# Kernel tuning notes

Hardware: AMD Instinct MI355X
Metric: run time of the kernel (lower is better)

## Reference

```python
import jax, jax.numpy as jnp
import numpy as np
import math

D = 1024
H = 16

def _new_gelu(x):
    return 0.5 * x * (1.0 + jnp.tanh(math.sqrt(2.0 / math.pi) * (x + 0.044715 * x ** 3)))

def _layer_norm(x, w):
    mu = jnp.mean(x, axis=-1, keepdims=True)
    var = jnp.var(x, axis=-1, keepdims=True)
    return (x - mu) * jax.lax.rsqrt(var + 1e-5) * w

def setup_inputs() -> dict:
    key = jax.random.key(0)
    ks = jax.random.split(key, 8)
    B, T = 2, 2048
    s = lambda fan_in: 1.0 / math.sqrt(fan_in)
    return {
        "x": jax.random.normal(ks[0], (B, T, D), jnp.float32),
        "ln1_w": jnp.ones((D,), jnp.float32),
        "attn_w": jax.random.normal(ks[1], (D, 3 * D), jnp.float32) * s(D),
        "attn_b": jnp.zeros((3 * D,), jnp.float32),
        "proj_w": jax.random.normal(ks[2], (D, D), jnp.float32) * s(D),
        "proj_b": jnp.zeros((D,), jnp.float32),
        "ln2_w": jnp.ones((D,), jnp.float32),
        "li1_w": jax.random.normal(ks[3], (D, 4 * D), jnp.float32) * s(D),
        "li1_b": jnp.zeros((4 * D,), jnp.float32),
        "li2_w": jax.random.normal(ks[4], (4 * D, D), jnp.float32) * s(4 * D),
        "li2_b": jnp.zeros((D,), jnp.float32),
    }

def reference(x, ln1_w, attn_w, attn_b, proj_w, proj_b, ln2_w, li1_w, li1_b, li2_w, li2_b):
    B, T, C = x.shape
    Dh = C // H
    # --- causal self-attention on pre-LN input ---
    h = _layer_norm(x, ln1_w)
    qkv = h @ attn_w + attn_b                      # [B,T,3C]
    q, k, v = jnp.split(qkv, 3, axis=-1)
    q = q.reshape(B, T, H, Dh)
    k = k.reshape(B, T, H, Dh)
    v = v.reshape(B, T, H, Dh)
    # NOTE: faithful to source — scale is 1/sqrt(BATCH), not 1/sqrt(head_dim)
    scale = 1.0 / math.sqrt(B)
    scores = jnp.einsum('bthd,bshd->bhts', q, k) * scale   # [B,H,T,T]
    causal = jnp.tril(jnp.ones((T, T), bool))
    scores = jnp.where(causal, scores, -jnp.inf)
    attn = jax.nn.softmax(scores, axis=-1)
    o = jnp.einsum('bhts,bshd->bthd', attn, v).reshape(B, T, C)
    x = x + o @ proj_w + proj_b
    # --- MLP ---
    h = _layer_norm(x, ln2_w)
    x = x + _new_gelu(h @ li1_w + li1_b) @ li2_w + li2_b
    return x
```

## Files before the change

kernel.cpp:

```cpp
#include <hip/hip_runtime.h>

typedef _Float16 f16;
typedef _Float16 f16x8 __attribute__((ext_vector_type(8)));
typedef _Float16 f16x4 __attribute__((ext_vector_type(4)));
typedef float    f32x4 __attribute__((ext_vector_type(4)));
typedef float    f32x16 __attribute__((ext_vector_type(16)));
typedef unsigned u32;
typedef unsigned u32x4 __attribute__((ext_vector_type(4)));

#define GAS __attribute__((address_space(1)))
#define LAS __attribute__((address_space(3)))

template <int N> struct IC { static constexpr int v = N; };

static __device__ __forceinline__ void gload_lds16(const void* g, void* l) {
    __builtin_amdgcn_global_load_lds((const GAS void*)g, (LAS void*)l, 16, 0, 0);
}

__global__ void wconv_t(const float* __restrict__ w, f16* __restrict__ wt, int K, int N) {
    __shared__ f16 t[32][33];
    const int tx = threadIdx.x, ty = threadIdx.y;
    const int n0 = blockIdx.x * 32, k0 = blockIdx.y * 32;
#pragma unroll
    for (int i = 0; i < 4; i++)
        t[ty + i * 8][tx] = (f16)w[(size_t)(k0 + ty + i * 8) * N + n0 + tx];
    __syncthreads();
#pragma unroll
    for (int i = 0; i < 4; i++)
        wt[(size_t)(n0 + ty + i * 8) * K + k0 + tx] = t[tx][ty + i * 8];
}

__global__ __launch_bounds__(256) void ln_kernel(const float* __restrict__ x,
                                                 const float* __restrict__ w,
                                                 f16* __restrict__ h) {
    const int row = blockIdx.x, tid = threadIdx.x;
    const float4 v = reinterpret_cast<const float4*>(x)[(size_t)row * 256 + tid];
    float s = v.x + v.y + v.z + v.w;
    float q = v.x * v.x + v.y * v.y + v.z * v.z + v.w * v.w;
#pragma unroll
    for (int m = 1; m < 64; m <<= 1) { s += __shfl_xor(s, m); q += __shfl_xor(q, m); }
    __shared__ float ss[4], qq[4];
    if ((tid & 63) == 0) { ss[tid >> 6] = s; qq[tid >> 6] = q; }
    __syncthreads();
    s = ss[0] + ss[1] + ss[2] + ss[3];
    q = qq[0] + qq[1] + qq[2] + qq[3];
    const float mu = s * (1.0f / 1024.0f);
    const float var = q * (1.0f / 1024.0f) - mu * mu;
    const float rs = rsqrtf(var + 1e-5f);
    const float4 wv = reinterpret_cast<const float4*>(w)[tid];
    f16x4 o;
    o[0] = (f16)((v.x - mu) * rs * wv.x);
    o[1] = (f16)((v.y - mu) * rs * wv.y);
    o[2] = (f16)((v.z - mu) * rs * wv.z);
    o[3] = (f16)((v.w - mu) * rs * wv.w);
    reinterpret_cast<f16x4*>(h)[(size_t)row * 256 + tid] = o;
}

__global__ __launch_bounds__(256) void vtrans(const f16* __restrict__ V, f16* __restrict__ Vt) {
    __shared__ f16 tl[64][72];
    const int tid = threadIdx.x;
    const int t0 = blockIdx.x * 64, bh = blockIdx.y;
    const int b = bh >> 4, hh = bh & 15;
    const int rr = tid >> 3, cc = (tid & 7) * 8;
#pragma unroll
    for (int p = 0; p < 2; p++) {
        f16x8 v = *(const f16x8*)(V + (size_t)(b * 2048 + t0 + p * 32 + rr) * 1024 + hh * 64 + cc);
#pragma unroll
        for (int j = 0; j < 8; j++) tl[p * 32 + rr][cc + j] = v[j];
    }
    __syncthreads();
#pragma unroll
    for (int p = 0; p < 2; p++) {
        const int d = p * 32 + rr;
        f16x8 o;
#pragma unroll
        for (int j = 0; j < 8; j++) o[j] = tl[cc + j][d];
        *(f16x8*)(Vt + (size_t)(bh * 64 + d) * 2048 + t0 + cc) = o;
    }
}

template <int EPI>
static __device__ __forceinline__ void gemm_epi(
    int gr, int gc, float v, int N, int gx,
    const float* bias, const float* res, void* outp,
    f16* oq, f16* ok, f16* ov, int bz, int BM) {
    if (EPI == 0) {
        if (gc < 1024)      oq[(size_t)gr * 1024 + gc]        = (f16)(v * 0.70710678118654752f);
        else if (gc < 2048) ok[(size_t)gr * 1024 + gc - 1024] = (f16)v;
        else                ov[(size_t)gr * 1024 + gc - 2048] = (f16)v;
    } else if (EPI == 1) {
        ((float*)outp)[(size_t)gr * N + gc] = v + res[(size_t)gr * N + gc];
    } else if (EPI == 2) {
        const float z = 0.7978845608028654f * (v + 0.044715f * v * v * v);
        const float t = 1.0f - 2.0f / (__builtin_amdgcn_exp2f(2.8853900817779268f * z) + 1.0f);
        ((f16*)outp)[(size_t)gr * N + gc] = (f16)(0.5f * v * (1.0f + t));
    } else {
        float* P = (float*)outp + (size_t)bz * ((size_t)gx * BM) * N;
        P[(size_t)gr * N + gc] = v;
    }
}

template <int EPI>
__global__ __launch_bounds__(512, 2) void gemm256(
    const f16* __restrict__ A, int lda,
    const f16* __restrict__ Bt, int ldb,
    const float* __restrict__ bias,
    const float* __restrict__ res,
    void* __restrict__ outp,
    f16* __restrict__ oq, f16* __restrict__ ok, f16* __restrict__ ov,
    int N, int K) {
    __shared__ alignas(16) f16 pool[8 * 8192];
    const int tid = threadIdx.x;
    const int lane = tid & 63, wv = tid >> 6;
    const int wr = wv >> 2, wc = wv & 3;
    const int m0 = blockIdx.x * 256, n0 = blockIdx.y * 256;
    const int l15 = lane & 15, lg = lane >> 4;
    const int swz = l15 & 7;

    f32x4 acc[8][4] = {};
    f16x8 bf[4][2];

    const int gcol16 = (tid & 7) ^ ((tid >> 3) & 7);
    const f16* aSrc[2][2];
    const f16* bSrc[2][2];
#pragma unroll
    for (int c = 0; c < 2; c++) {
        const int lr = c * 64 + (tid >> 3);
#pragma unroll
        for (int h = 0; h < 2; h++) {
            const int ar = ((lr >> 5) << 6) + h * 32 + (lr & 31);
            aSrc[c][h] = A + (size_t)(m0 + ar) * lda + gcol16 * 8;
            const int br = ((lr >> 6) << 7) + h * 64 + (lr & 63);
            bSrc[c][h] = Bt + (size_t)(n0 + br) * ldb + gcol16 * 8;
        }
    }
    f16* ldst = pool + tid * 8;

    auto stageQ = [&](int par, int qid, int kt) {
        f16* d = ldst + (par * 4 + qid) * 8192;
        if (qid >= 2) {
            gload_lds16(aSrc[0][qid - 2] + kt * 64, d);
            gload_lds16(aSrc[1][qid - 2] + kt * 64, d + 4096);
        } else {
            gload_lds16(bSrc[0][qid] + kt * 64, d);
            gload_lds16(bSrc[1][qid] + kt * 64, d + 4096);
        }
    };

    auto loadB = [&](int par) {
        const f16* bb = pool + par * 32768 + (wc & 1) * 8192 + (wc >> 1) * 4096 + l15 * 64;
#pragma unroll
        for (int ni = 0; ni < 4; ni++)
#pragma unroll
            for (int kk = 0; kk < 2; kk++)
                bf[ni][kk] = *(const f16x8*)(bb + ni * 1024 + (((kk * 4 + lg) ^ swz) * 8));
    };
    auto computeQ = [&](int par, auto qc) {
        constexpr int Q = decltype(qc)::v;
        const f16* ab = pool + par * 32768 + (2 + (Q & 1)) * 8192
                        + wr * 4096 + (Q >> 1) * 2048 + l15 * 64;
        f16x8 af[2][2];
#pragma unroll
        for (int mi2 = 0; mi2 < 2; mi2++)
#pragma unroll
            for (int kk = 0; kk < 2; kk++)
                af[mi2][kk] = *(const f16x8*)(ab + mi2 * 1024 + (((kk * 4 + lg) ^ swz) * 8));
        __builtin_amdgcn_s_setprio(1);
#pragma unroll
        for (int mi2 = 0; mi2 < 2; mi2++)
#pragma unroll
            for (int ni = 0; ni < 4; ni++)
#pragma unroll
                for (int kk = 0; kk < 2; kk++)
                    acc[Q * 2 + mi2][ni] = __builtin_amdgcn_mfma_f32_16x16x32_f16(
                        af[mi2][kk], bf[ni][kk], acc[Q * 2 + mi2][ni], 0, 0, 0);
        __builtin_amdgcn_s_setprio(0);
    };

#define VMW(n) asm volatile("s_waitcnt vmcnt(" #n ")" ::: "memory"); __builtin_amdgcn_s_barrier()

    const int nt = K >> 6;
    stageQ(0, 0, 0); stageQ(0, 1, 0); stageQ(0, 2, 0); stageQ(0, 3, 0);
    stageQ(1, 0, 1);
    VMW(6);

    for (int kt = 0; kt < nt - 2; ++kt) {
        const int par = kt & 1, parn = par ^ 1;
        stageQ(parn, 1, kt + 1); VMW(6); loadB(par); computeQ(par, IC<0>{});
        stageQ(parn, 2, kt + 1); VMW(6); computeQ(par, IC<1>{});
        stageQ(parn, 3, kt + 1); VMW(6); computeQ(par, IC<2>{});
        stageQ(par, 0, kt + 2);  VMW(6); computeQ(par, IC<3>{});
    }
    {
        const int kt = nt - 2, par = kt & 1, parn = par ^ 1;
        stageQ(parn, 1, kt + 1); VMW(6); loadB(par); computeQ(par, IC<0>{});
        stageQ(parn, 2, kt + 1); VMW(6); computeQ(par, IC<1>{});
        stageQ(parn, 3, kt + 1); VMW(6); computeQ(par, IC<2>{});
        VMW(4); computeQ(par, IC<3>{});
    }
    {
        const int par = (nt - 1) & 1;
        VMW(2); loadB(par); computeQ(par, IC<0>{});
        VMW(0); computeQ(par, IC<1>{});
        computeQ(par, IC<2>{});
        computeQ(par, IC<3>{});
    }
#undef VMW

#pragma unroll
    for (int mi = 0; mi < 8; mi++)
#pragma unroll
        for (int ni = 0; ni < 4; ni++) {
            const int gc = n0 + wc * 64 + ni * 16 + l15;
            const float bb = (EPI == 3) ? 0.0f : bias[gc];
#pragma unroll
            for (int r = 0; r < 4; r++) {
                const int gr = m0 + wr * 128 + mi * 16 + lg * 4 + r;
                gemm_epi<EPI>(gr, gc, acc[mi][ni][r] + bb, N, gridDim.x,
                              bias, res, outp, oq, ok, ov, blockIdx.z, 256);
            }
        }
}

template <int EPI>
__global__ __launch_bounds__(512) void gemm128(
    const f16* __restrict__ A, int lda,
    const f16* __restrict__ Bt, int ldb,
    const float* __restrict__ bias,
    const float* __restrict__ res,
    void* __restrict__ outp,
    f16* __restrict__ oq, f16* __restrict__ ok, f16* __restrict__ ov,
    int N, int K) {
    __shared__ alignas(16) f16 As[3][128 * 32];
    __shared__ alignas(16) f16 Bs[3][128 * 32];
    const int tid = threadIdx.x;
    const int lane = tid & 63, wv = tid >> 6;
    const int wr = wv >> 2, wc = wv & 3;
    const int m0 = blockIdx.x * 128, n0 = blockIdx.y * 128;
    const int l15 = lane & 15, lg = lane >> 4;

    f32x4 acc[4][2] = {};

    const int ar = tid >> 2;
    const int ac = (tid & 3) * 8;
    const size_t koff = (size_t)blockIdx.z * K;
    const f16* gA = A + (size_t)(m0 + ar) * lda + ac + koff;
    const f16* gB = Bt + (size_t)(n0 + ar) * ldb + ac + koff;
    char* lA0 = (char*)As + wv * 1024;
    char* lB0 = (char*)Bs + wv * 1024;

    auto stage = [&](int buf, int k0) {
        gload_lds16(gA + k0, lA0 + buf * 8192);
        gload_lds16(gB + k0, lB0 + buf * 8192);
    };
    auto compute = [&](int buf) {
        f16x8 af[4], bf[2];
#pragma unroll
        for (int i = 0; i < 4; i++)
            af[i] = *(const f16x8*)&As[buf][(wr * 64 + i * 16 + l15) * 32 + lg * 8];
#pragma unroll
        for (int n = 0; n < 2; n++)
            bf[n] = *(const f16x8*)&Bs[buf][(wc * 32 + n * 16 + l15) * 32 + lg * 8];
#pragma unroll
        for (int mi = 0; mi < 4; mi++)
#pragma unroll
            for (int ni = 0; ni < 2; ni++)
                acc[mi][ni] = __builtin_amdgcn_mfma_f32_16x16x32_f16(af[mi], bf[ni], acc[mi][ni], 0, 0, 0);
    };

    const int nk = K >> 5;
    stage(0, 0);
    if (nk > 1) {
        stage(1, 32);
        asm volatile("s_waitcnt vmcnt(2)" ::: "memory");
    } else {
        asm volatile("s_waitcnt vmcnt(0)" ::: "memory");
    }
    __builtin_amdgcn_s_barrier();

    for (int t = 0; t < nk; ++t) {
        const bool pref = (t + 2 < nk);
        if (pref) stage((t + 2) % 3, (t + 2) * 32);
        compute(t % 3);
        if (t + 1 < nk) {
            if (pref) asm volatile("s_waitcnt vmcnt(2)" ::: "memory");
            else      asm volatile("s_waitcnt vmcnt(0)" ::: "memory");
            __builtin_amdgcn_s_barrier();
        }
    }

#pragma unroll
    for (int mi = 0; mi < 4; mi++)
#pragma unroll
        for (int ni = 0; ni < 2; ni++) {
            const int gc = n0 + wc * 32 + ni * 16 + l15;
            const float bb = (EPI == 3) ? 0.0f : bias[gc];
#pragma unroll
            for (int r = 0; r < 4; r++) {
                const int gr = m0 + wr * 64 + mi * 16 + lg * 4 + r;
                gemm_epi<EPI>(gr, gc, acc[mi][ni][r] + bb, N, gridDim.x,
                              bias, res, outp, oq, ok, ov, blockIdx.z, 128);
            }
        }
}

__global__ __launch_bounds__(256) void kred(const float* __restrict__ p0,
                                            const float* __restrict__ p1,
                                            const float* __restrict__ bias,
                                            const float* __restrict__ res,
                                            float* __restrict__ out) {
    const size_t i = (size_t)blockIdx.x * 256 + threadIdx.x;
    const float4 a = ((const float4*)p0)[i];
    const float4 b = ((const float4*)p1)[i];
    const float4 r = ((const float4*)res)[i];
    const float4 w = ((const float4*)bias)[i & 255];
    float4 o;
    o.x = a.x + b.x + r.x + w.x;
    o.y = a.y + b.y + r.y + w.y;
    o.z = a.z + b.z + r.z + w.z;
    o.w = a.w + b.w + r.w + w.w;
    ((float4*)out)[i] = o;
}

__global__ __launch_bounds__(512) void attn_kernel(
    const f16* __restrict__ Q, const f16* __restrict__ Kb,
    const f16* __restrict__ Vt, f16* __restrict__ O) {
    __shared__ alignas(16) char pool[32768];
    const int tid = threadIdx.x, lane = tid & 63, w = tid >> 6;
    const int l31 = lane & 31, hi = lane >> 5;
    const int bx = blockIdx.x;
    const int qs = bx >> 5, bh = bx & 31;
    const int b = bh >> 4, hh = bh & 15;
    const int qtile = w * 8 + qs;
    const int q0 = qtile * 32;
    const int last = qtile >> 1;
    const int nk = ((56 + qs) >> 1) + 1;

    const f16* qrow = Q + (size_t)(b * 2048 + q0 + l31) * 1024 + hh * 64 + hi * 8;
    f16x8 qf[4];
#pragma unroll
    for (int s = 0; s < 4; s++) qf[s] = *(const f16x8*)(qrow + s * 16);

    f32x16 oacc[2] = {};
    float m = -3e38f, l = 0.0f;

    const int srow = tid >> 3, sslot = (tid & 7) ^ ((tid >> 3) & 7);
    const f16* kg = Kb + ((size_t)b * 2048 + srow) * 1024 + hh * 64 + sslot * 8;
    const f16* vg = Vt + ((size_t)bh * 64 + srow) * 2048 + sslot * 8;
    char* kld = pool + tid * 16;
    char* vld = pool + 8192 + tid * 16;

    auto stage = [&](int buf, int kt) {
        gload_lds16(kg + (size_t)kt * 65536, kld + buf * 16384);
        gload_lds16(vg + kt * 64, vld + buf * 16384);
    };

    const int rs = l31 & 7;

    auto tilestep = [&](int buf, bool diag) {
        const f16* Kbuf = (const f16*)(pool + buf * 16384);
        const f16* Vbuf = (const f16*)(pool + buf * 16384 + 8192);
        const bool doH1 = !diag || (qtile & 1);
        const int triH = qtile & 1;

        f16x8 k0[4], k1[4];
#pragma unroll
        for (int s = 0; s < 4; s++)
            k0[s] = *(const f16x8*)&Kbuf[l31 * 64 + (((s * 2 + hi) ^ rs) * 8)];
        if (doH1)
#pragma unroll
            for (int s = 0; s < 4; s++)
                k1[s] = *(const f16x8*)&Kbuf[(32 + l31) * 64 + (((s * 2 + hi) ^ rs) * 8)];

        f32x16 sacc0 = {}, sacc1 = {};
        __builtin_amdgcn_s_setprio(1);
#pragma unroll
        for (int s = 0; s < 4; s++)
            sacc0 = __builtin_amdgcn_mfma_f32_32x32x16_f16(k0[s], qf[s], sacc0, 0, 0, 0);
        if (doH1)
#pragma unroll
            for (int s = 0; s < 4; s++)
                sacc1 = __builtin_amdgcn_mfma_f32_32x32x16_f16(k1[s], qf[s], sacc1, 0, 0, 0);
        __builtin_amdgcn_s_setprio(0);

        if (diag) {
            if (triH == 0) {
#pragma unroll
                for (int r = 0; r < 16; r++) {
                    const int keyoff = (r & 3) + 8 * (r >> 2) + 4 * hi;
                    sacc0[r] = (keyoff > l31) ? -3e38f : sacc0[r];
                }
            } else {
#pragma unroll
                for (int r = 0; r < 16; r++) {
                    const int keyoff = (r & 3) + 8 * (r >> 2) + 4 * hi;
                    sacc1[r] = (keyoff > l31) ? -3e38f : sacc1[r];
                }
            }
        }
        float t8[8];
#pragma unroll
        for (int i = 0; i < 8; i++) t8[i] = fmaxf(sacc0[2 * i], sacc0[2 * i + 1]);
        if (doH1)
#pragma unroll
            for (int i = 0; i < 8; i++) t8[i] = fmaxf(t8[i], fmaxf(sacc1[2 * i], sacc1[2 * i + 1]));
#pragma unroll
        for (int i = 0; i < 4; i++) t8[i] = fmaxf(t8[i], t8[i + 4]);
        float tm = fmaxf(fmaxf(t8[0], t8[1]), fmaxf(t8[2], t8[3]));
        tm = fmaxf(tm, __shfl_xor(tm, 32));
        const bool up = tm > m + 8.0f;
        if (__any(up)) {
            const float mnew = up ? tm : m;
            const float alpha = __expf(m - mnew);
            m = mnew;
            l *= alpha;
#pragma unroll
            for (int r = 0; r < 16; r++) { oacc[0][r] *= alpha; oacc[1][r] *= alpha; }
        }
        const float mref = m * 1.44269504f;

        float psum = 0.0f;
        u32 wd[8];
        {
            float p[16];
#pragma unroll
            for (int r = 0; r < 16; r++)
                p[r] = __builtin_amdgcn_exp2f(sacc0[r] * 1.44269504f - mref);
            float s8[8];
#pragma unroll
            for (int i = 0; i < 8; i++) s8[i] = p[2 * i] + p[2 * i + 1];
#pragma unroll
            for (int i = 0; i < 4; i++) s8[i] = s8[i] + s8[i + 4];
            psum += (s8[0] + s8[1]) + (s8[2] + s8[3]);
#pragma unroll
            for (int i = 0; i < 8; i++)
                wd[i] = __builtin_bit_cast(u32, __builtin_amdgcn_cvt_pkrtz(p[2 * i], p[2 * i + 1]));
        }
        const u32 e0 = __shfl_xor(hi ? wd[0] : wd[2], 32);
        const u32 e1 = __shfl_xor(hi ? wd[1] : wd[3], 32);
        const u32 e2 = __shfl_xor(hi ? wd[4] : wd[6], 32);
        const u32 e3 = __shfl_xor(hi ? wd[5] : wd[7], 32);
        u32x4 c0, c1;
        c0[0] = hi ? e0 : wd[0]; c0[1] = hi ? e1 : wd[1];
        c0[2] = hi ? wd[2] : e0; c0[3] = hi ? wd[3] : e1;
        c1[0] = hi ? e2 : wd[4]; c1[1] = hi ? e3 : wd[5];
        c1[2] = hi ? wd[6] : e2; c1[3] = hi ? wd[7] : e3;
        const f16x8 pb00 = __builtin_bit_cast(f16x8, c0);
        const f16x8 pb01 = __builtin_bit_cast(f16x8, c1);

        f16x8 vfa, vfb;
        __builtin_amdgcn_s_setprio(1);
        vfa = *(const f16x8*)&Vbuf[l31 * 64 + ((hi ^ rs) * 8)];
        vfb = *(const f16x8*)&Vbuf[l31 * 64 + (((2 + hi) ^ rs) * 8)];
        oacc[0] = __builtin_amdgcn_mfma_f32_32x32x16_f16(vfa, pb00, oacc[0], 0, 0, 0);
        oacc[0] = __builtin_amdgcn_mfma_f32_32x32x16_f16(vfb, pb01, oacc[0], 0, 0, 0);
        vfa = *(const f16x8*)&Vbuf[(32 + l31) * 64 + ((hi ^ rs) * 8)];
        vfb = *(const f16x8*)&Vbuf[(32 + l31) * 64 + (((2 + hi) ^ rs) * 8)];
        oacc[1] = __builtin_amdgcn_mfma_f32_32x32x16_f16(vfa, pb00, oacc[1], 0, 0, 0);
        oacc[1] = __builtin_amdgcn_mfma_f32_32x32x16_f16(vfb, pb01, oacc[1], 0, 0, 0);
        __builtin_amdgcn_s_setprio(0);

        if (doH1) {
            float p[16];
#pragma unroll
            for (int r = 0; r < 16; r++)
                p[r] = __builtin_amdgcn_exp2f(sacc1[r] * 1.44269504f - mref);
            float s8[8];
#pragma unroll
            for (int i = 0; i < 8; i++) s8[i] = p[2 * i] + p[2 * i + 1];
#pragma unroll
            for (int i = 0; i < 4; i++) s8[i] = s8[i] + s8[i + 4];
            psum += (s8[0] + s8[1]) + (s8[2] + s8[3]);
#pragma unroll
            for (int i = 0; i < 8; i++)
                wd[i] = __builtin_bit_cast(u32, __builtin_amdgcn_cvt_pkrtz(p[2 * i], p[2 * i + 1]));
            const u32 f0 = __shfl_xor(hi ? wd[0] : wd[2], 32);
            const u32 f1 = __shfl_xor(hi ? wd[1] : wd[3], 32);
            const u32 f2 = __shfl_xor(hi ? wd[4] : wd[6], 32);
            const u32 f3 = __shfl_xor(hi ? wd[5] : wd[7], 32);
            u32x4 d0, d1;
            d0[0] = hi ? f0 : wd[0]; d0[1] = hi ? f1 : wd[1];
            d0[2] = hi ? wd[2] : f0; d0[3] = hi ? wd[3] : f1;
            d1[0] = hi ? f2 : wd[4]; d1[1] = hi ? f3 : wd[5];
            d1[2] = hi ? wd[6] : f2; d1[3] = hi ? wd[7] : f3;
            const f16x8 pb10 = __builtin_bit_cast(f16x8, d0);
            const f16x8 pb11 = __builtin_bit_cast(f16x8, d1);

            __builtin_amdgcn_s_setprio(1);
            vfa = *(const f16x8*)&Vbuf[l31 * 64 + (((4 + hi) ^ rs) * 8)];
            vfb = *(const f16x8*)&Vbuf[l31 * 64 + (((6 + hi) ^ rs) * 8)];
            oacc[0] = __builtin_amdgcn_mfma_f32_32x32x16_f16(vfa, pb10, oacc[0], 0, 0, 0);
            oacc[0] = __builtin_amdgcn_mfma_f32_32x32x16_f16(vfb, pb11, oacc[0], 0, 0, 0);
            vfa = *(const f16x8*)&Vbuf[(32 + l31) * 64 + (((4 + hi) ^ rs) * 8)];
            vfb = *(const f16x8*)&Vbuf[(32 + l31) * 64 + (((6 + hi) ^ rs) * 8)];
            oacc[1] = __builtin_amdgcn_mfma_f32_32x32x16_f16(vfa, pb10, oacc[1], 0, 0, 0);
            oacc[1] = __builtin_amdgcn_mfma_f32_32x32x16_f16(vfb, pb11, oacc[1], 0, 0, 0);
            __builtin_amdgcn_s_setprio(0);
        }
        psum += __shfl_xor(psum, 32);
        l += psum;
    };

    stage(0, 0);
    asm volatile("s_waitcnt vmcnt(0)" ::: "memory");
    __builtin_amdgcn_s_barrier();
    int buf = 0;
    for (int t = 0; t < nk; ++t) {
        if (t + 1 < nk) stage(buf ^ 1, t + 1);
        if (t <= last) tilestep(buf, t == last);
        asm volatile("s_waitcnt vmcnt(0)" ::: "memory");
        __builtin_amdgcn_s_barrier();
        buf ^= 1;
    }

    const float inv = 1.0f / l;
    f16* ot = (f16*)pool + (w & 3) * (32 * 72);
#pragma unroll
    for (int g = 0; g < 2; g++) {
        if ((w >> 2) == g) {
#pragma unroll
            for (int dt = 0; dt < 2; dt++)
#pragma unroll
                for (int r = 0; r < 16; r++) {
                    const int d = dt * 32 + (r & 3) + 8 * (r >> 2) + 4 * hi;
                    ot[l31 * 72 + d] = (f16)(oacc[dt][r] * inv);
                }
            asm volatile("s_waitcnt lgkmcnt(0)" ::: "memory");
#pragma unroll
            for (int i = 0; i < 4; i++) {
                const int row = i * 8 + (lane >> 3), col = (lane & 7) * 8;
                const f16x8 o8 = *(const f16x8*)&ot[row * 72 + col];
                *(f16x8*)(O + (size_t)(b * 2048 + q0 + row) * 1024 + hh * 64 + col) = o8;
            }
        }
        __syncthreads();
    }
}

extern "C" void kernel_launch(void* const* d_in, const int* in_sizes, int n_in,
                              void* d_out, int out_size, void* d_ws, size_t ws_size,
                              hipStream_t stream) {
    const float* x      = (const float*)d_in[0];
    const float* ln1_w  = (const float*)d_in[1];
    const float* attn_w = (const float*)d_in[2];
    const float* attn_b = (const float*)d_in[3];
    const float* proj_w = (const float*)d_in[4];
    const float* proj_b = (const float*)d_in[5];
    const float* ln2_w  = (const float*)d_in[6];
    const float* li1_w  = (const float*)d_in[7];
    const float* li1_b  = (const float*)d_in[8];
    const float* li2_w  = (const float*)d_in[9];
    const float* li2_b  = (const float*)d_in[10];
    float* out = (float*)d_out;

    char* ws = (char*)d_ws;
    size_t off = 0;
    auto alloc = [&](size_t bytes) { void* p = ws + off; off += (bytes + 255) & ~(size_t)255; return p; };
    f16* W1t = (f16*)alloc((size_t)3072 * 1024 * 2);
    f16* W2t = (f16*)alloc((size_t)1024 * 1024 * 2);
    f16* W3t = (f16*)alloc((size_t)4096 * 1024 * 2);
    f16* W4t = (f16*)alloc((size_t)1024 * 4096 * 2);
    f16* h   = (f16*)alloc((size_t)4096 * 1024 * 2);
    f16* Qb  = (f16*)alloc((size_t)4096 * 1024 * 2);
    f16* Kb  = (f16*)alloc((size_t)4096 * 1024 * 2);
    f16* Vb  = (f16*)alloc((size_t)4096 * 1024 * 2);
    f16* Vt  = (f16*)alloc((size_t)4096 * 1024 * 2);
    f16* Ob  = (f16*)alloc((size_t)4096 * 1024 * 2);
    float* x1 = (float*)alloc((size_t)4096 * 1024 * 4);
    float* P  = (float*)alloc((size_t)2 * 4096 * 1024 * 4);
    f16* Ab = Qb;

    dim3 b328(32, 8);
    wconv_t<<<dim3(96, 32),  b328, 0, stream>>>(attn_w, W1t, 1024, 3072);
    wconv_t<<<dim3(32, 32),  b328, 0, stream>>>(proj_w, W2t, 1024, 1024);
    wconv_t<<<dim3(128, 32), b328, 0, stream>>>(li1_w,  W3t, 1024, 4096);
    wconv_t<<<dim3(32, 128), b328, 0, stream>>>(li2_w,  W4t, 4096, 1024);

    ln_kernel<<<4096, 256, 0, stream>>>(x, ln1_w, h);
    gemm256<0><<<dim3(16, 12), 512, 0, stream>>>(h, 1024, W1t, 1024, attn_b, nullptr,
                                                 nullptr, Qb, Kb, Vb, 3072, 1024);
    vtrans<<<dim3(32, 32), 256, 0, stream>>>(Vb, Vt);
    attn_kernel<<<256, 512, 0, stream>>>(Qb, Kb, Vt, Ob);
    gemm128<1><<<dim3(32, 8), 512, 0, stream>>>(Ob, 1024, W2t, 1024, proj_b, x,
                                                x1, nullptr, nullptr, nullptr, 1024, 1024);
    ln_kernel<<<4096, 256, 0, stream>>>(x1, ln2_w, h);
    gemm256<2><<<dim3(16, 16), 512, 0, stream>>>(h, 1024, W3t, 1024, li1_b, nullptr,
                                                 Ab, nullptr, nullptr, nullptr, 4096, 1024);
    gemm128<3><<<dim3(32, 8, 2), 512, 0, stream>>>(Ab, 4096, W4t, 4096, nullptr, nullptr,
                                                   P, nullptr, nullptr, nullptr, 1024, 2048);
    kred<<<4096, 256, 0, stream>>>(P, P + (size_t)4096 * 1024, li2_b, x1, out);
}
```

Measured before the change: 246.3 us.

## Software-pipeline LDS fragment reads one quarter ahead of MFMA in gemm256

Restructures the gemm256 main loop so the A and B fragments for the next quarter (and the next k-tile's first quarter) are read from LDS before the current quarter's MFMAs issue. Global-to-LDS staging now runs three quarters ahead instead of one. LDS read latency is meant to hide behind matrix math rather than stall each quarter. This costs extra registers for the double-buffered fragments (bfN, afE, afO) under launch_bounds(512,2), and adds lgkmcnt(0) waits at every barrier.

After: 247.8 us. No clear change (+0.6%).

```diff
diff --git a/kernel.cpp b/kernel.cpp
--- a/kernel.cpp
+++ b/kernel.cpp
@@ -118,7 +118,7 @@
     const int swz = l15 & 7;
 
     f32x4 acc[8][4] = {};
-    f16x8 bf[4][2];
+    f16x8 bf[4][2], bfN[2][2], afE[2][2], afO[2][2];
 
     const int gcol16 = (tid & 7) ^ ((tid >> 3) & 7);
     const f16* aSrc[2][2];
@@ -147,24 +147,34 @@
         }
     };
 
-    auto loadB = [&](int par) {
+    auto rdBF01 = [&](int par, f16x8 (*dst)[2]) {
         const f16* bb = pool + par * 32768 + (wc & 1) * 8192 + (wc >> 1) * 4096 + l15 * 64;
 #pragma unroll
-        for (int ni = 0; ni < 4; ni++)
+        for (int ni = 0; ni < 2; ni++)
+#pragma unroll
+            for (int kk = 0; kk < 2; kk++)
+                dst[ni][kk] = *(const f16x8*)(bb + ni * 1024 + (((kk * 4 + lg) ^ swz) * 8));
+    };
+    auto rdBF23 = [&](int par) {
+        const f16* bb = pool + par * 32768 + (wc & 1) * 8192 + (wc >> 1) * 4096 + l15 * 64;
+#pragma unroll
+        for (int ni = 2; ni < 4; ni++)
 #pragma unroll
             for (int kk = 0; kk < 2; kk++)
                 bf[ni][kk] = *(const f16x8*)(bb + ni * 1024 + (((kk * 4 + lg) ^ swz) * 8));
     };
-    auto computeQ = [&](int par, auto qc) {
+    auto rdAF = [&](auto qc, int par, f16x8 (&af)[2][2]) {
         constexpr int Q = decltype(qc)::v;
         const f16* ab = pool + par * 32768 + (2 + (Q & 1)) * 8192
                         + wr * 4096 + (Q >> 1) * 2048 + l15 * 64;
-        f16x8 af[2][2];
 #pragma unroll
         for (int mi2 = 0; mi2 < 2; mi2++)
 #pragma unroll
             for (int kk = 0; kk < 2; kk++)
                 af[mi2][kk] = *(const f16x8*)(ab + mi2 * 1024 + (((kk * 4 + lg) ^ swz) * 8));
+    };
+    auto doMFMA = [&](auto qc, const f16x8 (&af)[2][2]) {
+        constexpr int Q = decltype(qc)::v;
         __builtin_amdgcn_s_setprio(1);
 #pragma unroll
         for (int mi2 = 0; mi2 < 2; mi2++)
@@ -177,35 +187,50 @@
         __builtin_amdgcn_s_setprio(0);
     };
 
-#define VMW(n) asm volatile("s_waitcnt vmcnt(" #n ")" ::: "memory"); __builtin_amdgcn_s_barrier()
+#define VMW6 { asm volatile("s_waitcnt vmcnt(6) lgkmcnt(0)" ::: "memory"); __builtin_amdgcn_s_barrier(); }
+#define VMW4 { asm volatile("s_waitcnt vmcnt(4) lgkmcnt(0)" ::: "memory"); __builtin_amdgcn_s_barrier(); }
+#define VMW2 { asm volatile("s_waitcnt vmcnt(2) lgkmcnt(0)" ::: "memory"); __builtin_amdgcn_s_barrier(); }
+#define VMW0 { asm volatile("s_waitcnt vmcnt(0) lgkmcnt(0)" ::: "memory"); __builtin_amdgcn_s_barrier(); }
+
+#define ITER(PARV, KT, STGA1, STGN, NXT, VW0, VW1, VW2, VW3)                   \
+    {                                                                          \
+        rdBF23(PARV); rdAF(IC<1>{}, PARV, afO);                                \
+        if (STGA1) stageQ((PARV) ^ 1, 3, (KT) + 1);                            \
+        VW0; doMFMA(IC<0>{}, afE);                                             \
+        rdAF(IC<2>{}, PARV, afE);                                              \
+        if (STGN) stageQ(PARV, 0, (KT) + 2);                                   \
+        VW1; doMFMA(IC<1>{}, afO);                                             \
+        rdAF(IC<3>{}, PARV, afO);                                              \
+        if (STGN) stageQ(PARV, 1, (KT) + 2);                                   \
+        VW2; doMFMA(IC<2>{}, afE);                                             \
+        if (NXT) { rdBF01((PARV) ^ 1, bfN); rdAF(IC<0>{}, (PARV) ^ 1, afE); }  \
+        if (STGN) stageQ(PARV, 2, (KT) + 2);                                   \
+        VW3; doMFMA(IC<3>{}, afO);                                             \
+        if (NXT) {                                                             \
+            bf[0][0] = bfN[0][0]; bf[0][1] = bfN[0][1];                        \
+            bf[1][0] = bfN[1][0]; bf[1][1] = bfN[1][1];                        \
+        }                                                                      \
+    }
 
     const int nt = K >> 6;
     stageQ(0, 0, 0); stageQ(0, 1, 0); stageQ(0, 2, 0); stageQ(0, 3, 0);
-    stageQ(1, 0, 1);
-    VMW(6);
+    stageQ(1, 0, 1); stageQ(1, 1, 1); stageQ(1, 2, 1);
+    VMW6;
+    rdBF01(0, bf);
+    rdAF(IC<0>{}, 0, afE);
 
     for (int kt = 0; kt < nt - 2; ++kt) {
-        const int par = kt & 1, parn = par ^ 1;
-        stageQ(parn, 1, kt + 1); VMW(6); loadB(par); computeQ(par, IC<0>{});
-        stageQ(parn, 2, kt + 1); VMW(6); computeQ(par, IC<1>{});
-        stageQ(parn, 3, kt + 1); VMW(6); computeQ(par, IC<2>{});
-        stageQ(par, 0, kt + 2);  VMW(6); computeQ(par, IC<3>{});
-    }
-    {
-        const int kt = nt - 2, par = kt & 1, parn = par ^ 1;
-        stageQ(parn, 1, kt + 1); VMW(6); loadB(par); computeQ(par, IC<0>{});
-        stageQ(parn, 2, kt + 1); VMW(6); computeQ(par, IC<1>{});
-        stageQ(parn, 3, kt + 1); VMW(6); computeQ(par, IC<2>{});
-        VMW(4); computeQ(par, IC<3>{});
-    }
-    {
-        const int par = (nt - 1) & 1;
-        VMW(2); loadB(par); computeQ(par, IC<0>{});
-        VMW(0); computeQ(par, IC<1>{});
-        computeQ(par, IC<2>{});
-        computeQ(par, IC<3>{});
-    }
-#undef VMW
+        const int par = kt & 1;
+        ITER(par, kt, 1, 1, 1, VMW6, VMW6, VMW6, VMW6);
+    }
+    ITER((nt - 2) & 1, nt - 2, 1, 0, 1, VMW6, VMW4, VMW2, VMW0);
+    ITER((nt - 1) & 1, nt - 1, 0, 0, 0, VMW0, VMW0, VMW0, VMW0);
+
+#undef ITER
+#undef VMW6
+#undef VMW4
+#undef VMW2
+#undef VMW0
 
 #pragma unroll
     for (int mi = 0; mi < 8; mi++)
```
